# Performance work log

Hardware: AMD Instinct MI355X
Metric: run time of the kernel (lower is better)

Reference implementation:

```python
import jax, jax.numpy as jnp
import numpy as np

NEG_INF = -1e9

def apply_rope(x, positions, head_dim, theta):
    # x: [B, S, H, Dh]; positions: [S] int32
    half = head_dim // 2
    fraction = (2.0 / head_dim) * jnp.arange(half, dtype=jnp.float32)  # [Dh/2]
    timescale = theta ** fraction
    angle = positions.astype(jnp.float32)[:, None] / timescale  # [S, Dh/2]
    sin = jnp.sin(angle)[None, :, None, :]  # [1,S,1,Dh/2]
    cos = jnp.cos(angle)[None, :, None, :]
    x1, x2 = jnp.split(x, 2, axis=-1)
    out = jnp.concatenate([x1 * cos - x2 * sin, x2 * cos + x1 * sin], axis=-1)
    return out.astype(x.dtype)

def setup_inputs() -> dict:
    key = jax.random.key(0)
    B, S, D = 2, 2048, 2048
    Q, N, H = 16, 4, 128
    ks = jax.random.split(key, 5)
    scale = 1.0 / np.sqrt(D)
    return {
        "x": jax.random.normal(ks[0], (B, S, D), dtype=jnp.float32),
        "positions": jnp.arange(S, dtype=jnp.int32),
        "Wq": jax.random.normal(ks[1], (Q, D, H), dtype=jnp.float32) * scale,
        "Wk": jax.random.normal(ks[2], (N, D, H), dtype=jnp.float32) * scale,
        "Wv": jax.random.normal(ks[3], (N, D, H), dtype=jnp.float32) * scale,
        "Wo": jax.random.normal(ks[4], (Q, H, D), dtype=jnp.float32) * scale,
    }

def reference(x, positions, Wq, Wk, Wv, Wo):
    head_dim = Wq.shape[-1]
    theta = 10000.0
    head_repeats = Wq.shape[0] // Wk.shape[0]  # GQA repeat factor

    q_BSQH = jnp.einsum('BSD,QDH->BSQH', x, Wq)
    q_BSQH = apply_rope(q_BSQH, positions, head_dim, theta)
    k_BTNH = jnp.einsum('BSD,NDH->BSNH', x, Wk)
    k_BTNH = apply_rope(k_BTNH, positions, head_dim, theta)
    v_BTNH = jnp.einsum('BSD,NDH->BSNH', x, Wv)

    k_BTQH = jnp.repeat(k_BTNH, head_repeats, axis=2)
    v_BTQH = jnp.repeat(v_BTNH, head_repeats, axis=2)

    scores_BQST = jnp.einsum('BSQH,BTQH->BQST', q_BSQH, k_BTQH) / jnp.sqrt(
        jnp.asarray(head_dim, dtype=x.dtype))
    S = q_BSQH.shape[1]
    causal = jnp.tril(jnp.ones((1, 1, S, S), dtype=jnp.bool_))
    scores_BQST = jnp.where(causal, scores_BQST, NEG_INF)
    weights_BQST = jax.nn.softmax(scores_BQST, axis=-1)
    out_BSQH = jnp.einsum('BQST,BTQH->BSQH', weights_BQST, v_BTQH)
    o_BSD = jnp.einsum('BSQH,QHD->BSD', out_BSQH, Wo)
    return o_BSD
```

## Files before the change

kernel.cpp:

```cpp
#include <hip/hip_runtime.h>
#include <math.h>

#define BB 2
#define SS 2048
#define DD 2048
#define QH 16
#define NKV 4
#define HD 128
#define REP 4
#define NEG_INF_F (-1e9f)

typedef __bf16 bfrag __attribute__((ext_vector_type(8)));
typedef float  ffrag __attribute__((ext_vector_type(4)));

__device__ inline unsigned short f2bf(float f) {
    unsigned u = __builtin_bit_cast(unsigned, f);
    u += 0x7fff + ((u >> 16) & 1);
    return (unsigned short)(u >> 16);
}
__device__ inline float bf2f(unsigned short u) {
    unsigned v = (unsigned)u << 16;
    return __builtin_bit_cast(float, v);
}
__device__ inline bfrag ld_frag(const unsigned short* p) {
    uint4 u = *(const uint4*)p;
    return __builtin_bit_cast(bfrag, u);
}
__device__ inline void async16(const void* g, void* l) {
    __builtin_amdgcn_global_load_lds(
        (const __attribute__((address_space(1))) unsigned int*)g,
        (__attribute__((address_space(3))) unsigned int*)l, 16, 0, 0);
}
__device__ inline unsigned pkbf(float a, float b) {
    unsigned short ua = __builtin_bit_cast(unsigned short, (__bf16)a);
    unsigned short ub = __builtin_bit_cast(unsigned short, (__bf16)b);
    return (unsigned)ua | ((unsigned)ub << 16);
}

__global__ __launch_bounds__(256) void prep_kernel(
    const float* __restrict__ x, unsigned short* __restrict__ xb,
    const float* __restrict__ Wq, const float* __restrict__ Wk,
    const float* __restrict__ Wv, const float* __restrict__ Wo,
    unsigned short* __restrict__ Wqkvt, unsigned short* __restrict__ Wot)
{
    __shared__ float tile[32][33];
    const int blk = blockIdx.x;
    const int tid = threadIdx.x;

    if (blk < 4096) {
        const int i = blk * 2048 + tid * 8;
        float4 a = *(const float4*)(x + i);
        float4 b = *(const float4*)(x + i + 4);
        unsigned short o[8];
        o[0] = f2bf(a.x); o[1] = f2bf(a.y); o[2] = f2bf(a.z); o[3] = f2bf(a.w);
        o[4] = f2bf(b.x); o[5] = f2bf(b.y); o[6] = f2bf(b.z); o[7] = f2bf(b.w);
        *(uint4*)(xb + i) = *(uint4*)o;
        return;
    }

    const float* in;
    unsigned short* out;
    int R, C, bx, by;
    if (blk < 10240) {
        const int lw = blk - 4096;
        const int z  = lw >> 8;
        const int r  = lw & 255;
        bx = r & 3; by = r >> 2;
        R = 2048; C = 128;
        if (z < 16)      { in = Wq + (size_t)z * 2048 * 128;
                           out = Wqkvt + (size_t)z * 128 * 2048; }
        else if (z < 20) { in = Wk + (size_t)(z - 16) * 2048 * 128;
                           out = Wqkvt + (size_t)(16 + (z - 16)) * 128 * 2048; }
        else             { in = Wv + (size_t)(z - 20) * 2048 * 128;
                           out = Wqkvt + (size_t)(20 + (z - 20)) * 128 * 2048; }
    } else {
        const int lw = blk - 10240;
        bx = lw & 63; by = lw >> 6;
        R = 2048; C = 2048;
        in = Wo; out = Wot;
    }
    const int c0 = bx * 32, r0 = by * 32;
    const int tx = tid & 31, ty = tid >> 5;
    #pragma unroll
    for (int k = 0; k < 4; ++k)
        tile[ty + 8 * k][tx] = in[(size_t)(r0 + ty + 8 * k) * C + c0 + tx];
    __syncthreads();
    #pragma unroll
    for (int k = 0; k < 4; ++k)
        out[(size_t)(c0 + ty + 8 * k) * R + r0 + tx] =
            f2bf(tile[tx][ty + 8 * k]);
}

__global__ __launch_bounds__(256) void gemm_bt_kernel(
    const unsigned short* __restrict__ A,
    const unsigned short* __restrict__ Bt,
    unsigned short* __restrict__ q_out, unsigned short* __restrict__ k_out,
    unsigned short* __restrict__ vt_out, float* __restrict__ f_out,
    int mode)
{
    const int m0 = blockIdx.x * 128;
    const int n0 = blockIdx.y * 128;
    const int tid  = threadIdx.x;
    const int w    = tid >> 6, lane = tid & 63;
    const int l16  = lane & 15, quad = lane >> 4;
    const int wm = (w >> 1) * 64, wn = (w & 1) * 64;

    __shared__ unsigned short As[128 * 32];
    __shared__ unsigned short Bs[128 * 32];

    ffrag acc[4][4];
    #pragma unroll
    for (int mi = 0; mi < 4; ++mi)
        #pragma unroll
        for (int ni = 0; ni < 4; ++ni)
            acc[mi][ni] = (ffrag){0.f, 0.f, 0.f, 0.f};

    for (int k0 = 0; k0 < 2048; k0 += 32) {
        __syncthreads();
        #pragma unroll
        for (int j = 0; j < 2; ++j) {
            const int i   = (j * 4 + w) * 64 + lane;
            const int row = i >> 2, seg = i & 3;
            async16(&A [(size_t)(m0 + row) * 2048 + k0 + seg * 8],
                    (char*)As + i * 16);
            async16(&Bt[(size_t)(n0 + row) * 2048 + k0 + seg * 8],
                    (char*)Bs + i * 16);
        }
        __syncthreads();

        bfrag af[4], bfr[4];
        #pragma unroll
        for (int mi = 0; mi < 4; ++mi)
            af[mi] = ld_frag(&As[(wm + mi * 16 + l16) * 32 + quad * 8]);
        #pragma unroll
        for (int ni = 0; ni < 4; ++ni)
            bfr[ni] = ld_frag(&Bs[(wn + ni * 16 + l16) * 32 + quad * 8]);
        #pragma unroll
        for (int mi = 0; mi < 4; ++mi)
            #pragma unroll
            for (int ni = 0; ni < 4; ++ni)
                acc[mi][ni] = __builtin_amdgcn_mfma_f32_16x16x32_bf16(
                    af[mi], bfr[ni], acc[mi][ni], 0, 0, 0);
    }

    if (mode == 0) {
        #pragma unroll
        for (int mi = 0; mi < 4; ++mi)
            #pragma unroll
            for (int ni = 0; ni < 4; ++ni) {
                const int col = n0 + wn + ni * 16 + l16;
                #pragma unroll
                for (int r = 0; r < 4; ++r) {
                    const int row = m0 + wm + mi * 16 + quad * 4 + r;
                    f_out[(size_t)row * 2048 + col] = acc[mi][ni][r];
                }
            }
    } else if (n0 < 2560) {
        unsigned short* dst;
        int colbase, stride;
        if (n0 < 2048)      { dst = q_out; colbase = n0;        stride = 2048; }
        else                { dst = k_out; colbase = n0 - 2048; stride = 512;  }
        #pragma unroll
        for (int mi = 0; mi < 4; ++mi)
            #pragma unroll
            for (int ni = 0; ni < 4; ++ni) {
                const int col = colbase + wn + ni * 16 + l16;
                #pragma unroll
                for (int r = 0; r < 4; ++r) {
                    const int row = m0 + wm + mi * 16 + quad * 4 + r;
                    dst[(size_t)row * stride + col] = f2bf(acc[mi][ni][r]);
                }
            }
    } else {
        const int c3 = n0 - 2560;
        #pragma unroll
        for (int mi = 0; mi < 4; ++mi)
            #pragma unroll
            for (int ni = 0; ni < 4; ++ni) {
                const int col = c3 + wn + ni * 16 + l16;
                const int nh = col >> 7, h = col & 127;
                const int row0 = m0 + wm + mi * 16 + quad * 4;
                const int b = row0 >> 11, s = row0 & 2047;
                unsigned short pk[4];
                #pragma unroll
                for (int r = 0; r < 4; ++r) pk[r] = f2bf(acc[mi][ni][r]);
                *(uint2*)&vt_out[(((size_t)b * NKV + nh) * HD + h) * SS + s] =
                    *(uint2*)pk;
            }
    }
}

__global__ void rope_kernel(unsigned short* __restrict__ q,
                            unsigned short* __restrict__ k,
                            const int* __restrict__ positions)
{
    const int qpairs = BB * SS * QH * 64;
    const int kpairs = BB * SS * NKV * 64;
    int idx = blockIdx.x * blockDim.x + threadIdx.x;
    unsigned short* base;
    int nh;
    if (idx < qpairs) { base = q; nh = QH; }
    else {
        idx -= qpairs;
        if (idx >= kpairs) return;
        base = k; nh = NKV;
    }
    const int hh   = idx & 63;
    const int rest = idx >> 6;
    const int head = rest % nh;
    const int bs   = rest / nh;
    const int s    = bs % SS;

    unsigned short* p = base + ((size_t)bs * nh + head) * HD;
    const float pos = (float)positions[s];
    const float inv_ts = powf(10000.0f, -(float)hh * (1.0f / 64.0f));
    const float angle = pos * inv_ts;
    const float sn = sinf(angle), cs = cosf(angle);
    const float sc_ = (nh == QH) ? 0.08838834764831845f : 1.0f;
    const float x1 = bf2f(p[hh]), x2 = bf2f(p[hh + 64]);
    p[hh]      = f2bf((x1 * cs - x2 * sn) * sc_);
    p[hh + 64] = f2bf((x2 * cs + x1 * sn) * sc_);
}

__global__ __launch_bounds__(512, 4) void attn_kernel(
    const unsigned short* __restrict__ qb,
    const unsigned short* __restrict__ kb,
    const unsigned short* __restrict__ vt,
    unsigned short* __restrict__ o)
{
    int f = blockIdx.y * 8 + blockIdx.x;
    f = (f & 7) * 32 + (f >> 3);
    const int bh = f >> 3;
    const int bx = f & 7;

    const int b  = bh / QH, qh = bh % QH;
    const int n  = qh / REP;

    const int tid  = threadIdx.x;
    const int w    = tid >> 6;
    const int lane = tid & 63;
    const int l16  = lane & 15;
    const int quad = lane >> 4;
    const int sw   = l16 & 7;

    __shared__ unsigned short Ks[2][2][64][64];
    __shared__ unsigned short Vs[2][128][64];
    __shared__ unsigned short Ps[8][16][64];

    const unsigned short* kbase = kb + (size_t)b * (SS * NKV * HD) + n * HD;
    const unsigned short* vbase = vt + ((size_t)b * NKV + n) * HD * SS;

    for (int ph = 0; ph < 2; ++ph) {
        const int super = ph == 0 ? (15 - bx) : bx;
        const int s0    = super * 128;
        const int rbase = s0 + w * 16 + quad * 4;
        const int thr   = s0 + w * 16 + l16;
        const int dlim  = s0 + ((w >> 2) << 6);

        bfrag qf[4];
        {
            const unsigned short* qp =
                qb + ((size_t)(b * SS + s0 + w * 16 + l16) * QH + qh) * HD
                   + quad * 8;
            #pragma unroll
            for (int c = 0; c < 4; ++c) qf[c] = ld_frag(qp + c * 32);
        }
        ffrag oacc[8];
        #pragma unroll
        for (int t = 0; t < 8; ++t) oacc[t] = (ffrag){0.f, 0.f, 0.f, 0.f};
        float mr = -1e30f, lr = 0.0f;

        #pragma unroll
        for (int j = 0; j < 2; ++j) {
            const int s = j * 512 + tid;
            {   const int cc = s >> 9, t = (s >> 3) & 63;
                const int sl = (s & 7) ^ (t & 7);
                async16(kbase + (size_t)t * (NKV * HD) + cc * 64 + sl * 8,
                        (char*)&Ks[0][0][0][0] + s * 16);
            }
            {   const int h = s >> 3, sl = (s & 7) ^ (h & 7);
                async16(vbase + (size_t)h * SS + sl * 8,
                        (char*)&Vs[0][0][0] + s * 16);
            }
        }
        __syncthreads();

        int p = 0;
        for (int t0 = 0; t0 <= s0 + 64; t0 += 64, p ^= 1) {
            if (t0 <= s0) {
                const int tn = t0 + 64;
                #pragma unroll
                for (int j = 0; j < 2; ++j) {
                    const int s = j * 512 + tid;
                    {   const int cc = s >> 9, t = (s >> 3) & 63;
                        const int sl = (s & 7) ^ (t & 7);
                        async16(kbase + (size_t)(tn + t) * (NKV * HD)
                                      + cc * 64 + sl * 8,
                                (char*)&Ks[p ^ 1][0][0][0] + s * 16);
                    }
                    {   const int h = s >> 3, sl = (s & 7) ^ (h & 7);
                        async16(vbase + (size_t)h * SS + tn + sl * 8,
                                (char*)&Vs[p ^ 1][0][0] + s * 16);
                    }
                }
            }

            if (t0 <= dlim) {
                ffrag sc[4];
                #pragma unroll
                for (int t = 0; t < 4; ++t)
                    sc[t] = (ffrag){0.f, 0.f, 0.f, 0.f};
                __builtin_amdgcn_s_setprio(1);
                #pragma unroll
                for (int c = 0; c < 4; ++c) {
                    const int cc = c >> 1, cb = (c & 1) * 4;
                    #pragma unroll
                    for (int t = 0; t < 4; ++t) {
                        bfrag kfr = ld_frag(
                            &Ks[p][cc][t * 16 + l16][((cb + quad) ^ sw) * 8]);
                        sc[t] = __builtin_amdgcn_mfma_f32_16x16x32_bf16(
                            kfr, qf[c], sc[t], 0, 0, 0);
                    }
                }
                __builtin_amdgcn_s_setprio(0);

                if (t0 == dlim) {
                    #pragma unroll
                    for (int t = 0; t < 4; ++t) {
                        const int col0 = t0 + t * 16 + quad * 4;
                        #pragma unroll
                        for (int r = 0; r < 4; ++r)
                            if (col0 + r > thr) sc[t][r] = NEG_INF_F;
                    }
                }

                float tmax;
                {
                    float a0 = fmaxf(fmaxf(sc[0][0], sc[0][1]),
                                     fmaxf(sc[0][2], sc[0][3]));
                    float a1 = fmaxf(fmaxf(sc[1][0], sc[1][1]),
                                     fmaxf(sc[1][2], sc[1][3]));
                    float a2 = fmaxf(fmaxf(sc[2][0], sc[2][1]),
                                     fmaxf(sc[2][2], sc[2][3]));
                    float a3 = fmaxf(fmaxf(sc[3][0], sc[3][1]),
                                     fmaxf(sc[3][2], sc[3][3]));
                    tmax = fmaxf(fmaxf(a0, a1), fmaxf(a2, a3));
                }
                tmax = fmaxf(tmax, __shfl_xor(tmax, 16));
                tmax = fmaxf(tmax, __shfl_xor(tmax, 32));

                if (__any(tmax > mr + 8.0f)) {
                    const float mnew  = fmaxf(mr, tmax);
                    const float alpha = __expf(mr - mnew);
                    lr *= alpha;
                    mr = mnew;
                    #pragma unroll
                    for (int r = 0; r < 4; ++r) {
                        const float ar =
                            __shfl(alpha, (lane & 48) | (quad * 4 + r));
                        #pragma unroll
                        for (int t = 0; t < 8; ++t) oacc[t][r] *= ar;
                    }
                }

                float ps = 0.f;
                #pragma unroll
                for (int t = 0; t < 4; ++t) {
                    const float p0 = __expf(sc[t][0] - mr);
                    const float p1 = __expf(sc[t][1] - mr);
                    const float p2 = __expf(sc[t][2] - mr);
                    const float p3 = __expf(sc[t][3] - mr);
                    ps += (p0 + p1) + (p2 + p3);
                    uint2 pk2;
                    pk2.x = pkbf(p0, p1);
                    pk2.y = pkbf(p2, p3);
                    const int sl = (2 * t + (quad >> 1)) ^ sw;
                    *(uint2*)&Ps[w][l16][sl * 8 + (quad & 1) * 4] = pk2;
                }
                ps += __shfl_xor(ps, 16);
                ps += __shfl_xor(ps, 32);
                lr += ps;

                __builtin_amdgcn_s_setprio(1);
                #pragma unroll
                for (int c = 0; c < 2; ++c) {
                    bfrag pf = ld_frag(
                        &Ps[w][l16][((c * 4 + quad) ^ sw) * 8]);
                    #pragma unroll
                    for (int t = 0; t < 8; ++t) {
                        bfrag vf = ld_frag(
                            &Vs[p][t * 16 + l16][((c * 4 + quad) ^ sw) * 8]);
                        oacc[t] = __builtin_amdgcn_mfma_f32_16x16x32_bf16(
                            pf, vf, oacc[t], 0, 0, 0);
                    }
                }
                __builtin_amdgcn_s_setprio(0);
            }

            __syncthreads();
        }

        #pragma unroll
        for (int r = 0; r < 4; ++r) {
            const float lrr  = __shfl(lr, (lane & 48) | (quad * 4 + r));
            const float invl = 1.0f / lrr;
            const int row = rbase + r;
            unsigned short* op = o + ((size_t)(b * SS + row) * QH + qh) * HD;
            #pragma unroll
            for (int t = 0; t < 8; ++t)
                op[t * 16 + l16] = f2bf(oacc[t][r] * invl);
        }
    }
}

extern "C" void kernel_launch(void* const* d_in, const int* in_sizes, int n_in,
                              void* d_out, int out_size, void* d_ws,
                              size_t ws_size, hipStream_t stream)
{
    const float* x         = (const float*)d_in[0];
    const int*   positions = (const int*)d_in[1];
    const float* Wq        = (const float*)d_in[2];
    const float* Wk        = (const float*)d_in[3];
    const float* Wv        = (const float*)d_in[4];
    const float* Wo        = (const float*)d_in[5];
    float* out = (float*)d_out;

    char* ws = (char*)d_ws;
    unsigned short* xb    = (unsigned short*)ws;
    unsigned short* Wqkvt = (unsigned short*)(ws + (16u << 20));
    unsigned short* Wot   = (unsigned short*)(ws + (28u << 20));
    unsigned short* qbf   = (unsigned short*)(ws + (36u << 20));
    unsigned short* kbf   = (unsigned short*)(ws + (52u << 20));
    unsigned short* vtb   = (unsigned short*)(ws + (56u << 20));
    unsigned short* opre  = xb;

    prep_kernel<<<14336, 256, 0, stream>>>(x, xb, Wq, Wk, Wv, Wo, Wqkvt, Wot);

    gemm_bt_kernel<<<dim3(32, 24), 256, 0, stream>>>(
        xb, Wqkvt, qbf, kbf, vtb, nullptr, 1);

    const int pairs = BB * SS * (QH + NKV) * 64;
    rope_kernel<<<(pairs + 255) / 256, 256, 0, stream>>>(qbf, kbf, positions);

    dim3 g2(8, BB * QH);
    attn_kernel<<<g2, 512, 0, stream>>>(qbf, kbf, vtb, opre);

    gemm_bt_kernel<<<dim3(32, 16), 256, 0, stream>>>(
        opre, Wot, nullptr, nullptr, nullptr, out, 0);
}
```

Measured before the change: 365.0 us.

## Deepen GEMM K-tile to 64 with swizzle; shrink attention blocks to 64-row tiles

The projection GEMM now stages 64-wide K slices with an XOR-swizzled shared layout and runs two MFMA sub-steps per barrier, halving the number of sync points and cutting LDS bank conflicts. The attention kernel moves from 512-thread blocks covering 128 query rows to 256-thread blocks covering 64 rows, with twice as many blocks. This removes the per-wave diagonal limit and changes the P buffer to a padded, unswizzled layout. Smaller attention tiles mean K/V is reloaded by more blocks in exchange for finer causal work balance and simpler control flow.

```diff
diff --git a/kernel.cpp b/kernel.cpp
--- a/kernel.cpp
+++ b/kernel.cpp
@@ -104,9 +104,10 @@
     const int w    = tid >> 6, lane = tid & 63;
     const int l16  = lane & 15, quad = lane >> 4;
     const int wm = (w >> 1) * 64, wn = (w & 1) * 64;
-
-    __shared__ unsigned short As[128 * 32];
-    __shared__ unsigned short Bs[128 * 32];
+    const int sw8 = l16 & 7;
+
+    __shared__ unsigned short As[128 * 64];
+    __shared__ unsigned short Bs[128 * 64];
 
     ffrag acc[4][4];
     #pragma unroll
@@ -115,32 +116,38 @@
         for (int ni = 0; ni < 4; ++ni)
             acc[mi][ni] = (ffrag){0.f, 0.f, 0.f, 0.f};
 
-    for (int k0 = 0; k0 < 2048; k0 += 32) {
+    for (int k0 = 0; k0 < 2048; k0 += 64) {
         __syncthreads();
         #pragma unroll
-        for (int j = 0; j < 2; ++j) {
-            const int i   = (j * 4 + w) * 64 + lane;
-            const int row = i >> 2, seg = i & 3;
-            async16(&A [(size_t)(m0 + row) * 2048 + k0 + seg * 8],
+        for (int j = 0; j < 4; ++j) {
+            const int i   = j * 256 + tid;
+            const int row = i >> 3;
+            const int sl  = (i & 7) ^ (row & 7);
+            async16(&A [(size_t)(m0 + row) * 2048 + k0 + sl * 8],
                     (char*)As + i * 16);
-            async16(&Bt[(size_t)(n0 + row) * 2048 + k0 + seg * 8],
+            async16(&Bt[(size_t)(n0 + row) * 2048 + k0 + sl * 8],
                     (char*)Bs + i * 16);
         }
         __syncthreads();
 
-        bfrag af[4], bfr[4];
-        #pragma unroll
-        for (int mi = 0; mi < 4; ++mi)
-            af[mi] = ld_frag(&As[(wm + mi * 16 + l16) * 32 + quad * 8]);
-        #pragma unroll
-        for (int ni = 0; ni < 4; ++ni)
-            bfr[ni] = ld_frag(&Bs[(wn + ni * 16 + l16) * 32 + quad * 8]);
-        #pragma unroll
-        for (int mi = 0; mi < 4; ++mi)
+        #pragma unroll
+        for (int c = 0; c < 2; ++c) {
+            bfrag af[4], bfr[4];
+            #pragma unroll
+            for (int mi = 0; mi < 4; ++mi)
+                af[mi] = ld_frag(&As[(wm + mi * 16 + l16) * 64
+                                     + (((c * 4 + quad) ^ sw8) * 8)]);
             #pragma unroll
             for (int ni = 0; ni < 4; ++ni)
-                acc[mi][ni] = __builtin_amdgcn_mfma_f32_16x16x32_bf16(
-                    af[mi], bfr[ni], acc[mi][ni], 0, 0, 0);
+                bfr[ni] = ld_frag(&Bs[(wn + ni * 16 + l16) * 64
+                                      + (((c * 4 + quad) ^ sw8) * 8)]);
+            #pragma unroll
+            for (int mi = 0; mi < 4; ++mi)
+                #pragma unroll
+                for (int ni = 0; ni < 4; ++ni)
+                    acc[mi][ni] = __builtin_amdgcn_mfma_f32_16x16x32_bf16(
+                        af[mi], bfr[ni], acc[mi][ni], 0, 0, 0);
+        }
     }
 
     if (mode == 0) {
@@ -222,16 +229,16 @@
     p[hh + 64] = f2bf((x2 * cs + x1 * sn) * sc_);
 }
 
-__global__ __launch_bounds__(512, 4) void attn_kernel(
+__global__ __launch_bounds__(256, 2) void attn_kernel(
     const unsigned short* __restrict__ qb,
     const unsigned short* __restrict__ kb,
     const unsigned short* __restrict__ vt,
     unsigned short* __restrict__ o)
 {
-    int f = blockIdx.y * 8 + blockIdx.x;
-    f = (f & 7) * 32 + (f >> 3);
-    const int bh = f >> 3;
-    const int bx = f & 7;
+    int f = blockIdx.y * 16 + blockIdx.x;
+    f = (f & 7) * 64 + (f >> 3);
+    const int bh = f >> 4;
+    const int bx = f & 15;
 
     const int b  = bh / QH, qh = bh % QH;
     const int n  = qh / REP;
@@ -245,17 +252,16 @@
 
     __shared__ unsigned short Ks[2][2][64][64];
     __shared__ unsigned short Vs[2][128][64];
-    __shared__ unsigned short Ps[8][16][64];
+    __shared__ unsigned short Ps[4][16][72];
 
     const unsigned short* kbase = kb + (size_t)b * (SS * NKV * HD) + n * HD;
     const unsigned short* vbase = vt + ((size_t)b * NKV + n) * HD * SS;
 
     for (int ph = 0; ph < 2; ++ph) {
-        const int super = ph == 0 ? (15 - bx) : bx;
-        const int s0    = super * 128;
+        const int tile = ph == 0 ? (31 - bx) : bx;
+        const int s0 = tile * 64;
         const int rbase = s0 + w * 16 + quad * 4;
-        const int thr   = s0 + w * 16 + l16;
-        const int dlim  = s0 + ((w >> 2) << 6);
+        const int thr   = w * 16 + l16;
 
         bfrag qf[4];
         {
@@ -271,8 +277,8 @@
         float mr = -1e30f, lr = 0.0f;
 
         #pragma unroll
-        for (int j = 0; j < 2; ++j) {
-            const int s = j * 512 + tid;
+        for (int j = 0; j < 4; ++j) {
+            const int s = j * 256 + tid;
             {   const int cc = s >> 9, t = (s >> 3) & 63;
                 const int sl = (s & 7) ^ (t & 7);
                 async16(kbase + (size_t)t * (NKV * HD) + cc * 64 + sl * 8,
@@ -286,12 +292,12 @@
         __syncthreads();
 
         int p = 0;
-        for (int t0 = 0; t0 <= s0 + 64; t0 += 64, p ^= 1) {
-            if (t0 <= s0) {
+        for (int t0 = 0; t0 <= s0; t0 += 64, p ^= 1) {
+            if (t0 + 64 <= s0) {
                 const int tn = t0 + 64;
                 #pragma unroll
-                for (int j = 0; j < 2; ++j) {
-                    const int s = j * 512 + tid;
+                for (int j = 0; j < 4; ++j) {
+                    const int s = j * 256 + tid;
                     {   const int cc = s >> 9, t = (s >> 3) & 63;
                         const int sl = (s & 7) ^ (t & 7);
                         async16(kbase + (size_t)(tn + t) * (NKV * HD)
@@ -305,97 +311,93 @@
                 }
             }
 
-            if (t0 <= dlim) {
-                ffrag sc[4];
-                #pragma unroll
-                for (int t = 0; t < 4; ++t)
-                    sc[t] = (ffrag){0.f, 0.f, 0.f, 0.f};
-                __builtin_amdgcn_s_setprio(1);
-                #pragma unroll
-                for (int c = 0; c < 4; ++c) {
-                    const int cc = c >> 1, cb = (c & 1) * 4;
+            ffrag sc[4];
+            #pragma unroll
+            for (int t = 0; t < 4; ++t) sc[t] = (ffrag){0.f, 0.f, 0.f, 0.f};
+            __builtin_amdgcn_s_setprio(1);
+            #pragma unroll
+            for (int c = 0; c < 4; ++c) {
+                const int cc = c >> 1, cb = (c & 1) * 4;
+                #pragma unroll
+                for (int t = 0; t < 4; ++t) {
+                    bfrag kfr = ld_frag(
+                        &Ks[p][cc][t * 16 + l16][((cb + quad) ^ sw) * 8]);
+                    sc[t] = __builtin_amdgcn_mfma_f32_16x16x32_bf16(
+                        kfr, qf[c], sc[t], 0, 0, 0);
+                }
+            }
+            __builtin_amdgcn_s_setprio(0);
+
+            const bool diag = (t0 == s0);
+            if (diag) {
+                #pragma unroll
+                for (int t = 0; t < 4; ++t) {
+                    const int col0 = t * 16 + quad * 4;
                     #pragma unroll
-                    for (int t = 0; t < 4; ++t) {
-                        bfrag kfr = ld_frag(
-                            &Ks[p][cc][t * 16 + l16][((cb + quad) ^ sw) * 8]);
-                        sc[t] = __builtin_amdgcn_mfma_f32_16x16x32_bf16(
-                            kfr, qf[c], sc[t], 0, 0, 0);
-                    }
-                }
-                __builtin_amdgcn_s_setprio(0);
-
-                if (t0 == dlim) {
+                    for (int r = 0; r < 4; ++r)
+                        if (col0 + r > thr) sc[t][r] = NEG_INF_F;
+                }
+            }
+
+            float tmax;
+            {
+                float a0 = fmaxf(fmaxf(sc[0][0], sc[0][1]),
+                                 fmaxf(sc[0][2], sc[0][3]));
+                float a1 = fmaxf(fmaxf(sc[1][0], sc[1][1]),
+                                 fmaxf(sc[1][2], sc[1][3]));
+                float a2 = fmaxf(fmaxf(sc[2][0], sc[2][1]),
+                                 fmaxf(sc[2][2], sc[2][3]));
+                float a3 = fmaxf(fmaxf(sc[3][0], sc[3][1]),
+                                 fmaxf(sc[3][2], sc[3][3]));
+                tmax = fmaxf(fmaxf(a0, a1), fmaxf(a2, a3));
+            }
+            tmax = fmaxf(tmax, __shfl_xor(tmax, 16));
+            tmax = fmaxf(tmax, __shfl_xor(tmax, 32));
+
+            if (__any(tmax > mr + 8.0f)) {
+                const float mnew  = fmaxf(mr, tmax);
+                const float alpha = __expf(mr - mnew);
+                lr *= alpha;
+                mr = mnew;
+                #pragma unroll
+                for (int r = 0; r < 4; ++r) {
+                    const float ar =
+                        __shfl(alpha, (lane & 48) | (quad * 4 + r));
                     #pragma unroll
-                    for (int t = 0; t < 4; ++t) {
-                        const int col0 = t0 + t * 16 + quad * 4;
-                        #pragma unroll
-                        for (int r = 0; r < 4; ++r)
-                            if (col0 + r > thr) sc[t][r] = NEG_INF_F;
-                    }
-                }
-
-                float tmax;
-                {
-                    float a0 = fmaxf(fmaxf(sc[0][0], sc[0][1]),
-                                     fmaxf(sc[0][2], sc[0][3]));
-                    float a1 = fmaxf(fmaxf(sc[1][0], sc[1][1]),
-                                     fmaxf(sc[1][2], sc[1][3]));
-                    float a2 = fmaxf(fmaxf(sc[2][0], sc[2][1]),
-                                     fmaxf(sc[2][2], sc[2][3]));
-                    float a3 = fmaxf(fmaxf(sc[3][0], sc[3][1]),
-                                     fmaxf(sc[3][2], sc[3][3]));
-                    tmax = fmaxf(fmaxf(a0, a1), fmaxf(a2, a3));
-                }
-                tmax = fmaxf(tmax, __shfl_xor(tmax, 16));
-                tmax = fmaxf(tmax, __shfl_xor(tmax, 32));
-
-                if (__any(tmax > mr + 8.0f)) {
-                    const float mnew  = fmaxf(mr, tmax);
-                    const float alpha = __expf(mr - mnew);
-                    lr *= alpha;
-                    mr = mnew;
-                    #pragma unroll
-                    for (int r = 0; r < 4; ++r) {
-                        const float ar =
-                            __shfl(alpha, (lane & 48) | (quad * 4 + r));
-                        #pragma unroll
-                        for (int t = 0; t < 8; ++t) oacc[t][r] *= ar;
-                    }
-                }
-
-                float ps = 0.f;
-                #pragma unroll
-                for (int t = 0; t < 4; ++t) {
-                    const float p0 = __expf(sc[t][0] - mr);
-                    const float p1 = __expf(sc[t][1] - mr);
-                    const float p2 = __expf(sc[t][2] - mr);
-                    const float p3 = __expf(sc[t][3] - mr);
-                    ps += (p0 + p1) + (p2 + p3);
-                    uint2 pk2;
-                    pk2.x = pkbf(p0, p1);
-                    pk2.y = pkbf(p2, p3);
-                    const int sl = (2 * t + (quad >> 1)) ^ sw;
-                    *(uint2*)&Ps[w][l16][sl * 8 + (quad & 1) * 4] = pk2;
-                }
-                ps += __shfl_xor(ps, 16);
-                ps += __shfl_xor(ps, 32);
-                lr += ps;
-
-                __builtin_amdgcn_s_setprio(1);
-                #pragma unroll
-                for (int c = 0; c < 2; ++c) {
-                    bfrag pf = ld_frag(
-                        &Ps[w][l16][((c * 4 + quad) ^ sw) * 8]);
-                    #pragma unroll
-                    for (int t = 0; t < 8; ++t) {
-                        bfrag vf = ld_frag(
-                            &Vs[p][t * 16 + l16][((c * 4 + quad) ^ sw) * 8]);
-                        oacc[t] = __builtin_amdgcn_mfma_f32_16x16x32_bf16(
-                            pf, vf, oacc[t], 0, 0, 0);
-                    }
-                }
-                __builtin_amdgcn_s_setprio(0);
-            }
+                    for (int t = 0; t < 8; ++t) oacc[t][r] *= ar;
+                }
+            }
+
+            float ps = 0.f;
+            #pragma unroll
+            for (int t = 0; t < 4; ++t) {
+                const float p0 = __expf(sc[t][0] - mr);
+                const float p1 = __expf(sc[t][1] - mr);
+                const float p2 = __expf(sc[t][2] - mr);
+                const float p3 = __expf(sc[t][3] - mr);
+                ps += (p0 + p1) + (p2 + p3);
+                uint2 pk2;
+                pk2.x = pkbf(p0, p1);
+                pk2.y = pkbf(p2, p3);
+                *(uint2*)&Ps[w][l16][t * 16 + quad * 4] = pk2;
+            }
+            ps += __shfl_xor(ps, 16);
+            ps += __shfl_xor(ps, 32);
+            lr += ps;
+
+            __builtin_amdgcn_s_setprio(1);
+            #pragma unroll
+            for (int c = 0; c < 2; ++c) {
+                bfrag pf = ld_frag(&Ps[w][l16][c * 32 + quad * 8]);
+                #pragma unroll
+                for (int t = 0; t < 8; ++t) {
+                    bfrag vf = ld_frag(
+                        &Vs[p][t * 16 + l16][((c * 4 + quad) ^ sw) * 8]);
+                    oacc[t] = __builtin_amdgcn_mfma_f32_16x16x32_bf16(
+                        pf, vf, oacc[t], 0, 0, 0);
+                }
+            }
+            __builtin_amdgcn_s_setprio(0);
 
             __syncthreads();
         }
@@ -442,8 +444,8 @@
     const int pairs = BB * SS * (QH + NKV) * 64;
     rope_kernel<<<(pairs + 255) / 256, 256, 0, stream>>>(qbf, kbf, positions);
 
-    dim3 g2(8, BB * QH);
-    attn_kernel<<<g2, 512, 0, stream>>>(qbf, kbf, vtb, opre);
+    dim3 g2(16, BB * QH);
+    attn_kernel<<<g2, 256, 0, stream>>>(qbf, kbf, vtb, opre);
 
     gemm_bt_kernel<<<dim3(32, 16), 256, 0, stream>>>(
         opre, Wot, nullptr, nullptr, nullptr, out, 0);
```

New measurement: 324.8 us. 1.12x faster.
